# Kernel optimization log

Hardware: AMD Instinct MI355X
Metric: run time of the kernel (lower is better)

Reference implementation:

```python
import jax, jax.numpy as jnp
import numpy as np

NEG = -jnp.inf


def _pipeline(logits, presence_penalties, frequency_penalties, repetition_penalties,
              temperatures, top_p, min_p, top_a, tfs, typical_p,
              epsilon_cutoff, eta_cutoff, smoothing_factor, smoothing_curve,
              prompt_tokens, output_tokens, top_k):
    N, V = logits.shape
    rows = jnp.arange(N)[:, None]
    cols = jnp.arange(V)[None, :]

    # ---- presence / frequency / repetition penalties (bincount via scatter-add) ----
    pbin = jnp.zeros((N, V + 1), jnp.int32).at[rows, prompt_tokens].add(1)[:, :V]
    obin = jnp.zeros((N, V + 1), jnp.int32).at[rows, output_tokens].add(1)[:, :V]
    seen = (pbin > 0) | (obin > 0)
    rp = jnp.where(seen, repetition_penalties[:, None], 1.0)
    logits = jnp.where(logits > 0, logits / rp, logits * rp)
    logits = logits - frequency_penalties[:, None] * obin.astype(logits.dtype)
    logits = logits - presence_penalties[:, None] * (obin > 0).astype(logits.dtype)

    # ---- temperature ----
    logits = logits / temperatures[:, None]

    # ---- top-k + top-p (sort ascending, mask, unsort) ----
    order = jnp.argsort(logits, axis=-1)               # ascending
    ls = jnp.take_along_axis(logits, order, axis=-1)
    kth_pos = (V - jnp.clip(top_k.astype(jnp.int32), 1, V))[:, None]
    kth_val = jnp.take_along_axis(ls, kth_pos, axis=1)
    ls = jnp.where(ls < kth_val, NEG, ls)
    cs = jnp.cumsum(jax.nn.softmax(ls, axis=-1), axis=-1)
    pmask = (cs <= (1.0 - top_p)[:, None]).at[:, -1].set(False)
    ls = jnp.where(pmask, NEG, ls)
    logits = jnp.take_along_axis(ls, jnp.argsort(order, axis=-1), axis=-1)

    # ---- tail-free sampling (sort descending, 2nd-derivative CDF cutoff) ----
    order_d = jnp.argsort(-logits, axis=-1)            # descending order of logits
    ls = jnp.take_along_axis(logits, order_d, axis=-1)
    probs = jax.nn.softmax(ls, axis=-1)
    d2 = jnp.abs(jnp.diff(jnp.diff(probs, axis=-1), axis=-1))   # (N, V-2)
    cdf = jnp.cumsum(d2 / jnp.sum(d2, axis=-1, keepdims=True), axis=-1)
    m = cdf > tfs[:, None]
    m = jnp.concatenate([jnp.zeros((N, 1), bool), m, jnp.ones((N, 1), bool)], axis=-1)
    ls = jnp.where(m, NEG, ls)
    logits = jnp.take_along_axis(ls, jnp.argsort(order_d, axis=-1), axis=-1)

    # ---- eta cutoff (entropy-adaptive threshold, always keep argmax) ----
    sl = jax.nn.log_softmax(logits, axis=-1)
    probs = jnp.exp(sl)
    sl_safe = jnp.where(probs > 0, sl, 0.0)            # nansum equivalent
    neg_ent = jnp.sum(probs * sl_safe, axis=-1)
    eps = jnp.minimum(eta_cutoff, jnp.sqrt(eta_cutoff) * jnp.exp(neg_ent))[:, None]
    top_idx = jnp.argmax(probs, axis=-1)[:, None]
    logits = jnp.where((probs < eps) & (cols != top_idx), NEG, logits)

    # ---- epsilon cutoff (absolute prob threshold, always keep argmax) ----
    probs = jax.nn.softmax(logits, axis=-1)
    top_idx = jnp.argmax(probs, axis=-1)[:, None]
    logits = jnp.where((probs < epsilon_cutoff[:, None]) & (cols != top_idx), NEG, logits)

    # ---- locally typical sampling ----
    sl = jax.nn.log_softmax(logits, axis=-1)
    probs = jnp.exp(sl)
    sl_safe = jnp.where(probs > 0, sl, 0.0)
    neg_ent = jnp.sum(probs * sl_safe, axis=-1, keepdims=True)
    dev = jnp.abs(neg_ent - sl)                        # surprisal deviation
    order_t = jnp.argsort(dev, axis=-1)
    rp2 = jnp.take_along_axis(probs, order_t, axis=-1)
    msort = (jnp.cumsum(rp2, axis=-1) >= typical_p[:, None]).at[:, 0].set(False)
    mask = jnp.zeros((N, V), bool).at[rows, order_t].set(msort)
    logits = jnp.where(mask, NEG, logits)

    # ---- quadratic (smoothing) sampling ----
    mx = jnp.max(logits, axis=-1, keepdims=True)
    finite = logits != NEG
    diff = jnp.where(finite, logits, mx) - mx          # finite everywhere
    kq = (3.0 - smoothing_curve[:, None]) / 2.0
    sq = (smoothing_curve[:, None] - 1.0) / 2.0
    sfc = smoothing_factor[:, None]
    trans = -(kq * sfc * diff ** 2) + sq * sfc * diff ** 3 + mx
    trans = jnp.where(finite, trans, logits)
    logits = jnp.where(sfc > 0, trans, logits)

    # ---- min-p ----
    probs = jax.nn.softmax(logits, axis=-1)
    top_prob = jnp.max(probs, axis=-1, keepdims=True)
    logits = jnp.where(probs < min_p[:, None] * top_prob, NEG, logits)

    # ---- top-a ----
    probs = jax.nn.softmax(logits, axis=-1)
    top_prob = jnp.max(probs, axis=-1, keepdims=True)
    logits = jnp.where(probs < top_a[:, None] * top_prob ** 2, NEG, logits)

    return logits


def setup_inputs() -> dict:
    N, V, PL, OL = 256, 50257, 512, 128
    ks = jax.random.split(jax.random.key(0), 17)
    u = lambda k, lo, hi: lo + (hi - lo) * jax.random.uniform(k, (N,), jnp.float32)
    return {
        "logits": 3.0 * jax.random.normal(ks[0], (N, V), jnp.float32),
        "prompt_tokens": jax.random.randint(ks[1], (N, PL), 0, V),
        "output_tokens": jax.random.randint(ks[2], (N, OL), 0, V),
        "presence_penalties": u(ks[3], 0.0, 0.5),
        "frequency_penalties": u(ks[4], 0.0, 0.5),
        "repetition_penalties": u(ks[5], 1.0, 1.3),
        "temperatures": u(ks[6], 0.5, 1.5),
        "top_p": u(ks[7], 0.85, 0.99),
        "top_k": jax.random.randint(ks[8], (N,), 1, 2048, dtype=jnp.int32),
        "min_p": u(ks[9], 0.0, 0.05),
        "top_a": u(ks[10], 0.0, 0.1),
        "tfs": u(ks[11], 0.95, 0.999),
        "typical_p": u(ks[12], 0.9, 0.999),
        "epsilon_cutoff": u(ks[13], 1e-5, 1e-4),
        "eta_cutoff": u(ks[14], 1e-5, 1e-4),
        "smoothing_factor": u(ks[15], 0.05, 0.25),
        "smoothing_curve": u(ks[16], 1.0, 2.0),
    }


def reference(logits, prompt_tokens, output_tokens, presence_penalties,
              frequency_penalties, repetition_penalties, temperatures, top_p,
              top_k, min_p, top_a, tfs, typical_p, epsilon_cutoff, eta_cutoff,
              smoothing_factor, smoothing_curve):
    return _pipeline(logits, presence_penalties, frequency_penalties,
                     repetition_penalties, temperatures, top_p, min_p, top_a,
                     tfs, typical_p, epsilon_cutoff, eta_cutoff,
                     smoothing_factor, smoothing_curve,
                     prompt_tokens, output_tokens, top_k)
```

## Files before the change

### kernel.cpp

```cpp
#include <hip/hip_runtime.h>
#include <stdint.h>

#define TPB 1024
#define NWAVE 16
#define MAXK 2304
#define NV4 13
#define BIG_NEG (-1.0e30f)

__device__ __forceinline__ uint32_t fkey(float x) {
  uint32_t s = __float_as_uint(x);
  return (s & 0x80000000u) ? ~s : (s | 0x80000000u);
}
__device__ __forceinline__ float fkey_inv(uint32_t u) {
  uint32_t s = (u & 0x80000000u) ? (u & 0x7fffffffu) : ~u;
  return __uint_as_float(s);
}
__device__ __forceinline__ unsigned long long shfl_xor_u64(unsigned long long v, int m) {
  uint32_t lo = (uint32_t)v, hi = (uint32_t)(v >> 32);
  lo = (uint32_t)__shfl_xor((int)lo, m, 64);
  hi = (uint32_t)__shfl_xor((int)hi, m, 64);
  return (((unsigned long long)hi) << 32) | lo;
}

struct TokMem { uint32_t obin[12568]; uint32_t seen[1600]; };
struct SortMem { unsigned long long kp[4096]; };
union __align__(16) U1 { TokMem tok; SortMem srt; };

__device__ __forceinline__ float block_sum1(float v, float* buf) {
  int lane = threadIdx.x & 63, wd = threadIdx.x >> 6;
#pragma unroll
  for (int off = 32; off > 0; off >>= 1) v += __shfl_down(v, off, 64);
  if (lane == 0) buf[wd] = v;
  __syncthreads();
  const float4* b4 = (const float4*)buf;
  float4 A = b4[0], B = b4[1], C = b4[2], D = b4[3];
  float r = A.x; r += A.y; r += A.z; r += A.w;
  r += B.x; r += B.y; r += B.z; r += B.w;
  r += C.x; r += C.y; r += C.z; r += C.w;
  r += D.x; r += D.y; r += D.z; r += D.w;
  return r;
}
__device__ __forceinline__ int block_count(int c, float* buf) {
  return (int)block_sum1((float)c, buf);
}

__device__ __forceinline__ float wbuf_prefix(const float* wbuf, int wd) {
  const float4* w4 = (const float4*)wbuf;
  float4 a = w4[0], b = w4[1], c = w4[2], d = w4[3];
  float t[16] = {a.x, a.y, a.z, a.w, b.x, b.y, b.z, b.w,
                 c.x, c.y, c.z, c.w, d.x, d.y, d.z, d.w};
  float base = 0.f;
#pragma unroll
  for (int i = 0; i < 16; ++i) base += (i < wd) ? t[i] : 0.f;
  return base;
}

__device__ void block_scan3(float* arr, int m, float* wbuf) {
  int tid = (int)threadIdx.x, lane = tid & 63, wd = tid >> 6;
  int b = tid * 3;
  __syncthreads();
  float a0 = (b < m) ? arr[b] : 0.f;
  float a1 = (b + 1 < m) ? arr[b + 1] : 0.f;
  float a2 = (b + 2 < m) ? arr[b + 2] : 0.f;
  float c1 = a0 + a1, c2 = c1 + a2;
  float t = c2, w = c2;
#pragma unroll
  for (int off = 1; off < 64; off <<= 1) {
    float x = __shfl_up(w, off, 64);
    if (lane >= off) w += x;
  }
  if (lane == 63) wbuf[wd] = w;
  __syncthreads();
  float base = wbuf_prefix(wbuf, wd);
  float excl = base + (w - t);
  if (b < m) arr[b] = a0 + excl;
  if (b + 1 < m) arr[b + 1] = c1 + excl;
  if (b + 2 < m) arr[b + 2] = c2 + excl;
  __syncthreads();
}

__device__ void block_scan3x2(float* A, float* B, int m, float* wbufA, float* wbufB) {
  int tid = (int)threadIdx.x, lane = tid & 63, wd = tid >> 6;
  int b = tid * 3;
  __syncthreads();
  float a0 = (b < m) ? A[b] : 0.f;
  float a1 = (b + 1 < m) ? A[b + 1] : 0.f;
  float a2 = (b + 2 < m) ? A[b + 2] : 0.f;
  float x0 = (b < m) ? B[b] : 0.f;
  float x1 = (b + 1 < m) ? B[b + 1] : 0.f;
  float x2 = (b + 2 < m) ? B[b + 2] : 0.f;
  float ca1 = a0 + a1, ca2 = ca1 + a2;
  float cx1 = x0 + x1, cx2 = cx1 + x2;
  float ta = ca2, wa = ca2, tx = cx2, wx = cx2;
#pragma unroll
  for (int off = 1; off < 64; off <<= 1) {
    float sa = __shfl_up(wa, off, 64);
    float sx = __shfl_up(wx, off, 64);
    if (lane >= off) { wa += sa; wx += sx; }
  }
  if (lane == 63) { wbufA[wd] = wa; wbufB[wd] = wx; }
  __syncthreads();
  float baseA = wbuf_prefix(wbufA, wd);
  float baseB = wbuf_prefix(wbufB, wd);
  float exA = baseA + (wa - ta), exB = baseB + (wx - tx);
  if (b < m) { A[b] = a0 + exA; B[b] = x0 + exB; }
  if (b + 1 < m) { A[b + 1] = ca1 + exA; B[b + 1] = cx1 + exB; }
  if (b + 2 < m) { A[b + 2] = ca2 + exA; B[b + 2] = cx2 + exB; }
  __syncthreads();
}

__device__ uint32_t wave_select_digit2k(const uint32_t* __restrict__ h, uint32_t* w_io) {
  int lane = threadIdx.x & 63;
  uint32_t w = *w_io;
  const int base = lane << 5;
  uint32_t lsum = 0;
#pragma unroll
  for (int t = 0; t < 8; ++t) {
    const int tt = (t + lane) & 7;
    const uint4 v = *(const uint4*)(h + base + tt * 4);
    lsum += v.x + v.y + v.z + v.w;
  }
  uint32_t W = lsum;
#pragma unroll
  for (int off = 1; off < 64; off <<= 1) {
    uint32_t x = (uint32_t)__shfl_down((int)W, off, 64);
    if (lane + off < 64) W += x;
  }
  uint32_t Wn = (uint32_t)__shfl_down((int)W, 1, 64);
  if (lane == 63) Wn = 0;
  const bool isb = (W >= w) && (Wn < w);
  int dloc = -1; uint32_t wloc = 0;
  if (isb) {
    uint32_t sfx = Wn;
#pragma unroll
    for (int t = 31; t >= 0; --t) {
      uint32_t c = h[base + t];
      uint32_t si = sfx + c;
      if (si >= w && sfx < w) { dloc = base + t; wloc = w - sfx; }
      sfx = si;
    }
  }
  unsigned long long bm = __ballot(dloc >= 0);
  int src = (int)__popcll(bm - 1ull);
  uint32_t d = (uint32_t)__shfl(dloc, src, 64);
  *w_io = (uint32_t)__shfl((int)wloc, src, 64);
  return d;
}

__device__ uint32_t wave_select_digit256(const uint32_t* __restrict__ h, uint32_t* w_io) {
  int lane = threadIdx.x & 63;
  uint32_t w = *w_io;
  const uint4 v = ((const uint4*)h)[lane];
  uint32_t c0 = v.x, c1 = v.y, c2 = v.z, c3 = v.w;
  uint32_t t0 = c0 + c1 + c2 + c3;
  uint32_t W = t0;
#pragma unroll
  for (int off = 1; off < 64; off <<= 1) {
    uint32_t x = (uint32_t)__shfl_down((int)W, off, 64);
    if (lane + off < 64) W += x;
  }
  uint32_t Wn = (uint32_t)__shfl_down((int)W, 1, 64);
  if (lane == 63) Wn = 0;
  uint32_t S0 = W, S1 = W - c0, S2 = S1 - c1, S3 = S2 - c2, S4 = Wn;
  int dloc = -1; uint32_t wloc = 0;
  if (S0 >= w && S1 < w) { dloc = 4 * lane + 0; wloc = w - S1; }
  if (S1 >= w && S2 < w) { dloc = 4 * lane + 1; wloc = w - S2; }
  if (S2 >= w && S3 < w) { dloc = 4 * lane + 2; wloc = w - S3; }
  if (S3 >= w && S4 < w) { dloc = 4 * lane + 3; wloc = w - S4; }
  unsigned long long bm = __ballot(dloc >= 0);
  int src = (int)__popcll(bm - 1ull);
  uint32_t d = (uint32_t)__shfl(dloc, src, 64);
  *w_io = (uint32_t)__shfl((int)wloc, src, 64);
  return d;
}

template <int NE, bool PING>
__device__ void hybrid_sort(unsigned long long* kp, unsigned long long* kb1, int n) {
  const int tid = (int)threadIdx.x;
  unsigned long long k[NE];
#pragma unroll
  for (int e = 0; e < NE; ++e) {
    int i = e * TPB + tid;
    k[e] = (i < n) ? kp[i] : ~0ull;
  }
  int pb = 0;
  for (int kk = 2; kk <= n; kk <<= 1) {
    for (int j = kk >> 1; j > 0; j >>= 1) {
      if (j >= TPB) {
        const int em = j / TPB;
#pragma unroll
        for (int e = 0; e < NE; ++e) {
          if ((e & em) == 0 && (e + em) < NE) {
            int e2 = e + em;
            int i = e * TPB + tid;
            bool up = ((i & kk) == 0);
            if ((k[e] > k[e2]) == up) {
              unsigned long long tk = k[e]; k[e] = k[e2]; k[e2] = tk;
            }
          }
        }
      } else if (j >= 64) {
        unsigned long long* kb = (PING && pb) ? kb1 : kp;
#pragma unroll
        for (int e = 0; e < NE; ++e) {
          int i = e * TPB + tid;
          if (i < n) kb[i] = k[e];
        }
        __syncthreads();
#pragma unroll
        for (int e = 0; e < NE; ++e) {
          int i = e * TPB + tid;
          if (i < n) {
            unsigned long long o = kb[i ^ j];
            bool up = ((i & kk) == 0);
            bool lower = ((i & j) == 0);
            bool takeMin = (lower == up);
            bool takeOther = takeMin ? (o < k[e]) : (o > k[e]);
            if (takeOther) k[e] = o;
          }
        }
        if (PING) pb ^= 1;
        else __syncthreads();
      } else {
#pragma unroll
        for (int e = 0; e < NE; ++e) {
          int i = e * TPB + tid;
          unsigned long long o = shfl_xor_u64(k[e], j);
          bool up = ((i & kk) == 0);
          bool lower = ((i & j) == 0);
          bool takeMin = (lower == up);
          bool takeOther = takeMin ? (o < k[e]) : (o > k[e]);
          if (takeOther) k[e] = o;
        }
      }
    }
  }
  __syncthreads();
#pragma unroll
  for (int e = 0; e < NE; ++e) {
    int i = e * TPB + tid;
    if (i < n) kp[i] = k[e];
  }
  __syncthreads();
}

__device__ __forceinline__ uint32_t penal_val(float l, int j, bool sn,
    const uint32_t* __restrict__ obin,
    float f_rep, float inv_rep, float f_freq, float f_pres, float inv_temp) {
  int ob = 0;
  if (sn) ob = (int)((obin[j >> 2] >> (8 * (j & 3))) & 255u);
  l = (l > 0.0f) ? (l * (sn ? inv_rep : 1.0f)) : (l * (sn ? f_rep : 1.0f));
  l = l - f_freq * (float)ob;
  l = l - ((ob > 0) ? f_pres : 0.0f);
  l = l * inv_temp;
  return fkey(l);
}
__device__ __forceinline__ uint32_t penal_key(float l, int j,
    const uint32_t* __restrict__ seen, const uint32_t* __restrict__ obin,
    float f_rep, float inv_rep, float f_freq, float f_pres, float inv_temp) {
  bool sn = (seen[j >> 5] >> (j & 31)) & 1u;
  return penal_val(l, j, sn, obin, f_rep, inv_rep, f_freq, f_pres, inv_temp);
}

#define FOR_ELEMS(...) do {                                                   \
    if (tid < head) { int j = tid; uint32_t u = uh; (void)j; (void)u; __VA_ARGS__; } \
    _Pragma("unroll")                                                         \
    for (int s4_ = 0; s4_ < NV4; ++s4_) {                                     \
      int iv_ = s4_ * TPB + tid;                                              \
      if (iv_ < nvec) {                                                       \
        int jb_ = head + 4 * iv_;                                             \
        { int j = jb_ + 0; uint32_t u = uk[s4_ * 4 + 0]; (void)j; (void)u; __VA_ARGS__; } \
        { int j = jb_ + 1; uint32_t u = uk[s4_ * 4 + 1]; (void)j; (void)u; __VA_ARGS__; } \
        { int j = jb_ + 2; uint32_t u = uk[s4_ * 4 + 2]; (void)j; (void)u; __VA_ARGS__; } \
        { int j = jb_ + 3; uint32_t u = uk[s4_ * 4 + 3]; (void)j; (void)u; __VA_ARGS__; } \
      }                                                                       \
    }                                                                         \
    if (tid < ntail) { int j = head + 4 * nvec + tid; uint32_t u = ut; (void)j; (void)u; __VA_ARGS__; } \
  } while (0)

#define COLLECT_ELEM do {                                                     \
    bool pk_ = (u >= kth_u);                                                  \
    unsigned long long bm_ = __ballot(pk_);                                   \
    if (bm_) {                                                                \
      uint32_t base_ = 0;                                                     \
      if (lane == 0) base_ = atomicAdd(&s_cnt, (uint32_t)__popcll(bm_));      \
      base_ = (uint32_t)__shfl((int)base_, 0, 64);                            \
      if (pk_) {                                                              \
        uint32_t pos_ = base_ + (uint32_t)__popcll(bm_ & ((1ull << (unsigned)lane) - 1ull)); \
        if (pos_ < MAXK)                                                      \
          kp[pos_] = (((unsigned long long)(~u)) << 16) | (unsigned long long)(uint32_t)j; \
      }                                                                       \
    }                                                                         \
  } while (0)

__global__ __launch_bounds__(TPB, 4)
void sampler_kernel(const float* __restrict__ logits,
                    const int* __restrict__ ptoks, const int* __restrict__ otoks,
                    const float* __restrict__ pres, const float* __restrict__ freq,
                    const float* __restrict__ rep, const float* __restrict__ temp,
                    const float* __restrict__ topp, const int* __restrict__ topk,
                    const float* __restrict__ minp, const float* __restrict__ topa,
                    const float* __restrict__ tfsv, const float* __restrict__ typp,
                    const float* __restrict__ epsc, const float* __restrict__ etac,
                    const float* __restrict__ smf, const float* __restrict__ smc,
                    float* __restrict__ out, int N, int V, int PL, int OL) {
  __shared__ U1 u1;
  __shared__ __align__(16) uint32_t s_hist2k[2048];
  __shared__ __align__(16) uint32_t s_h256[256];
  __shared__ float s_e[MAXK];
  __shared__ float s_p[MAXK];
  __shared__ float s_q[MAXK];
  __shared__ float s_r[MAXK];
  __shared__ unsigned long long kb1[2048];
  __shared__ __align__(16) float s_site[12][NWAVE];
  __shared__ uint32_t s_cnt;
  __shared__ int s_ilo, s_ihi;

  const int tid = (int)threadIdx.x;
  const int r = (int)blockIdx.x;
  const int wd = tid >> 6;
  const int lane = tid & 63;

  const float* lrow = logits + (size_t)r * V;
  float* orow = out + (size_t)r * V;

  {
    const uint4 z4 = make_uint4(0u, 0u, 0u, 0u);
    uint4* ob4 = (uint4*)u1.tok.obin;
    for (int i = tid; i < 3142; i += TPB) ob4[i] = z4;
    uint4* se4 = (uint4*)u1.tok.seen;
    for (int i = tid; i < 400; i += TPB) se4[i] = z4;
    uint4* h4 = (uint4*)s_hist2k;
    for (int i = tid; i < 512; i += TPB) h4[i] = z4;
    if (tid < 64) ((uint4*)s_h256)[tid] = z4;
  }
  if (tid == 0) s_cnt = 0;
  __syncthreads();
  for (int i = tid; i < PL; i += TPB) {
    int t = ptoks[(size_t)r * PL + i];
    if ((unsigned)t < (unsigned)V) atomicOr(&u1.tok.seen[t >> 5], 1u << (t & 31));
  }
  for (int i = tid; i < OL; i += TPB) {
    int t = otoks[(size_t)r * OL + i];
    if ((unsigned)t < (unsigned)V) {
      atomicOr(&u1.tok.seen[t >> 5], 1u << (t & 31));
      atomicAdd(&u1.tok.obin[t >> 2], 1u << (8 * (t & 3)));
    }
  }
  __syncthreads();

  const float f_pres = pres[r], f_freq = freq[r], f_rep = rep[r], f_temp = temp[r];
  const float f_topp = topp[r], f_minp = minp[r], f_topa = topa[r], f_tfs = tfsv[r];
  const float f_typp = typp[r], f_epsc = epsc[r], f_etac = etac[r];
  const float f_smf = smf[r], f_smc = smc[r];
  const float inv_rep = 1.0f / f_rep, inv_temp = 1.0f / f_temp;
  int k_topk = topk[r];
  if (k_topk < 1) k_topk = 1;
  if (k_topk > V) k_topk = V;

  const uint32_t* seenp = u1.tok.seen;
  const uint32_t* obinp = u1.tok.obin;

  uintptr_t ra = (uintptr_t)lrow;
  int head = (int)(((16u - (uint32_t)(ra & 15u)) & 15u) >> 2);
  if (head > V) head = V;
  const int nvec = (V - head) >> 2;
  const int ntail = V - head - (nvec << 2);

  uint32_t uk[NV4 * 4];
  uint32_t uh = 0, ut = 0;
#pragma unroll
  for (int s4 = 0; s4 < NV4; ++s4) {
    int iv = s4 * TPB + tid;
    uint32_t u0 = 0, u1k = 0, u2k = 0, u3 = 0;
    if (iv < nvec) {
      const float4 lv = *(const float4*)(lrow + head + 4 * iv);
      int jb = head + 4 * iv;
      uint32_t w0 = seenp[jb >> 5];
      uint32_t w1 = seenp[(jb >> 5) + 1];
      uint32_t sb = (uint32_t)(((((uint64_t)w1) << 32) | (uint64_t)w0) >> (jb & 31));
      u0 = penal_val(lv.x, jb + 0, (sb >> 0) & 1u, obinp, f_rep, inv_rep, f_freq, f_pres, inv_temp);
      u1k = penal_val(lv.y, jb + 1, (sb >> 1) & 1u, obinp, f_rep, inv_rep, f_freq, f_pres, inv_temp);
      u2k = penal_val(lv.z, jb + 2, (sb >> 2) & 1u, obinp, f_rep, inv_rep, f_freq, f_pres, inv_temp);
      u3 = penal_val(lv.w, jb + 3, (sb >> 3) & 1u, obinp, f_rep, inv_rep, f_freq, f_pres, inv_temp);
      atomicAdd(&s_hist2k[u0 >> 21], 1u);
      atomicAdd(&s_hist2k[u1k >> 21], 1u);
      atomicAdd(&s_hist2k[u2k >> 21], 1u);
      atomicAdd(&s_hist2k[u3 >> 21], 1u);
    }
    uk[s4 * 4 + 0] = u0; uk[s4 * 4 + 1] = u1k; uk[s4 * 4 + 2] = u2k; uk[s4 * 4 + 3] = u3;
  }
  if (tid < head) {
    uh = penal_key(lrow[tid], tid, seenp, obinp, f_rep, inv_rep, f_freq, f_pres, inv_temp);
    atomicAdd(&s_hist2k[uh >> 21], 1u);
  }
  if (tid < ntail) {
    int j = head + 4 * nvec + tid;
    ut = penal_key(lrow[j], j, seenp, obinp, f_rep, inv_rep, f_freq, f_pres, inv_temp);
    atomicAdd(&s_hist2k[ut >> 21], 1u);
  }

  {
    uintptr_t oa = (uintptr_t)orow;
    int ohead = (int)(((16u - (uint32_t)(oa & 15u)) & 15u) >> 2);
    if (ohead > V) ohead = V;
    int onvec = (V - ohead) >> 2;
    for (int j = tid; j < ohead; j += TPB) orow[j] = BIG_NEG;
    float4* o4 = (float4*)(orow + ohead);
    const float4 f4 = make_float4(BIG_NEG, BIG_NEG, BIG_NEG, BIG_NEG);
    for (int i = tid; i < onvec; i += TPB) o4[i] = f4;
    for (int j = ohead + (onvec << 2) + tid; j < V; j += TPB) orow[j] = BIG_NEG;
  }
  __syncthreads();

  uint32_t w = (uint32_t)k_topk;
  uint32_t d11 = wave_select_digit2k(s_hist2k, &w);
  FOR_ELEMS(if ((u >> 21) == d11) atomicAdd(&s_h256[(u >> 13) & 255u], 1u));
  __syncthreads();
  uint32_t d8 = wave_select_digit256(s_h256, &w);
  const uint32_t kth_u = (d11 << 21) | (d8 << 13);

  unsigned long long* kp = u1.srt.kp;
  FOR_ELEMS(COLLECT_ELEM);
  __syncthreads();
  int K = (int)s_cnt;
  if (K > MAXK) K = MAXK;

  {
    int n1 = 64; while (n1 < K) n1 <<= 1;
    for (int i = K + tid; i < n1; i += TPB) kp[i] = ~0ull;
    __syncthreads();
    if (n1 <= 1024) hybrid_sort<1, true>(kp, kb1, n1);
    else if (n1 == 2048) hybrid_sort<2, true>(kp, kb1, n1);
    else hybrid_sort<4, false>(kp, nullptr, n1);
  }

  {
    const uint32_t kth_inv = (uint32_t)(kp[k_topk - 1] >> 16);
    int c = 0;
    for (int i = tid; i < K; i += TPB)
      if ((uint32_t)(kp[i] >> 16) <= kth_inv) c++;
    K = block_count(c, s_site[10]);
  }

  const float m0 = fkey_inv(~(uint32_t)(kp[0] >> 16));

  for (int i = tid; i < K; i += TPB) {
    float v = fkey_inv(~(uint32_t)(kp[i] >> 16));
    float e = __expf(v - m0);
    s_e[i] = e; s_p[i] = e; s_q[i] = e * (v - m0);
  }
  block_scan3x2(s_p, s_q, K, s_site[8], s_site[9]);
  const float S = s_p[K - 1];

  {
    const float thS = (1.0f - f_topp) * S;
    int c = 0;
    for (int i = tid; i < K; i += TPB) {
      float ss = S - s_p[i] + s_e[i];
      if (i == 0 || ss > thS) c++;
    }
    K = block_count(c, s_site[0]);
  }

  {
    for (int i = tid; i < K; i += TPB) {
      float e0 = s_e[i];
      float e1 = (i + 1 < K) ? s_e[i + 1] : 0.f;
      float e2 = (i + 2 < K) ? s_e[i + 2] : 0.f;
      s_r[i] = fabsf((e2 - e1) - (e1 - e0));
    }
    block_scan3(s_r, K, s_site[7]);
    const float thT = f_tfs * s_r[K - 1];
    int c = 0;
    for (int i = tid; i < K; i += TPB)
      if (i == 0 || s_r[i - 1] <= thT) c++;
    K = block_count(c, s_site[1]);
  }

  {
    const float SD = s_p[K - 1];
    const float ne = s_q[K - 1] / SD - __logf(SD);
    const float eps = fminf(f_etac, sqrtf(f_etac) * __expf(ne));
    const float thD = eps * SD;
    int c = 0;
    for (int i = tid; i < K; i += TPB)
      if (i == 0 || s_e[i] >= thD) c++;
    K = block_count(c, s_site[2]);
  }

  {
    const float thE = f_epsc * s_p[K - 1];
    int c = 0;
    for (int i = tid; i < K; i += TPB)
      if (i == 0 || s_e[i] >= thE) c++;
    K = block_count(c, s_site[3]);
  }

  int i_lo = 0, i_hi = K - 1;
  {
    const float SF = s_p[K - 1];
    const float lseF = __logf(SF);
    const float ne = s_q[K - 1] / SF - lseF;
    const float vth = ne + lseF + m0;
    const float typSF = f_typp * SF;
    int cc = 0;
    for (int i = tid; i < K; i += TPB)
      if (fkey_inv(~(uint32_t)(kp[i] >> 16)) >= vth) cc++;
    const int c = block_count(cc, s_site[4]);
    const int nB = K - c;

    if (wd == 0) {
      auto keyAt = [&](int i) -> unsigned long long {
        unsigned long long kk = kp[i];
        float v = fkey_inv(~(uint32_t)(kk >> 16));
        return (((unsigned long long)fkey(fabsf(v - vth))) << 16) | (kk & 0xffffull);
      };
      auto splitFor = [&](int p) -> int {
        int alo = p - nB; if (alo < 0) alo = 0;
        int ahi = (p < c) ? p : c;
        while (alo < ahi) {
          int am = (alo + ahi + 1) >> 1;
          int tb = p - am;
          bool take = true;
          if (tb < nB) take = (keyAt(c - am) <= keyAt(c + tb));
          if (take) alo = am; else ahi = am - 1;
        }
        return alo;
      };
      auto massLess = [&](int p) -> bool {
        int a = splitFor(p);
        int b = p - a;
        float sum = s_p[c + b - 1] - ((c - a > 0) ? s_p[c - a - 1] : 0.f);
        return sum < typSF;
      };
      int plo = 0, phi = K;
      while (phi > plo) {
        int range = phi - plo;
        int stride = (range + 63) >> 6;
        int p = plo + stride * (lane + 1);
        bool q = false;
        if (p <= phi) q = massLess(p);
        unsigned long long bm = __ballot(q);
        int h = bm ? (63 - (int)__clzll(bm)) : -1;
        int nlo = (h >= 0) ? (plo + stride * (h + 1)) : plo;
        long long nf = (long long)plo + (long long)stride * (long long)(h + 2);
        int nhi = (nf <= (long long)phi) ? (int)nf - 1 : phi;
        plo = nlo; phi = nhi;
      }
      int L = plo;
      if (L < 1) L = 1;
      if (L > K) L = K;
      int a = splitFor(L);
      if (lane == 0) { s_ilo = c - a; s_ihi = c + (L - a) - 1; }
    }
    __syncthreads();
    i_lo = s_ilo; i_hi = s_ihi;
  }

  float S2;
  const float mx = fkey_inv(~(uint32_t)(kp[i_lo] >> 16));
  {
    const float kq = (3.0f - f_smc) * 0.5f;
    const float sq = (f_smc - 1.0f) * 0.5f;
    float pS = 0.f;
    for (int i = i_lo + tid; i <= i_hi; i += TPB) {
      float v = fkey_inv(~(uint32_t)(kp[i] >> 16));
      float d = v - mx;
      float tr = mx - (kq * f_smf) * (d * d) + (sq * f_smf) * ((d * d) * d);
      float v2 = (f_smf > 0.0f) ? tr : v;
      float e = __expf(v2 - mx);
      s_q[i] = e;
      s_r[i] = v2;
      if (e >= f_minp) pS += e;
    }
    S2 = block_sum1(pS, s_site[6]);
  }

  {
    const float thA = f_topa / S2;
    for (int i = i_lo + tid; i <= i_hi; i += TPB) {
      float e = s_q[i];
      if (e >= f_minp && e >= thA) {
        int idx = (int)(kp[i] & 0xffffull);
        orow[idx] = s_r[i];
      }
    }
  }
}

extern "C" void kernel_launch(void* const* d_in, const int* in_sizes, int n_in,
                              void* d_out, int out_size, void* d_ws, size_t ws_size,
                              hipStream_t stream) {
  const float* logits = (const float*)d_in[0];
  const int* ptoks = (const int*)d_in[1];
  const int* otoks = (const int*)d_in[2];
  const float* pres = (const float*)d_in[3];
  const float* freq = (const float*)d_in[4];
  const float* rep  = (const float*)d_in[5];
  const float* temp = (const float*)d_in[6];
  const float* topp = (const float*)d_in[7];
  const int*   topk = (const int*)d_in[8];
  const float* minp = (const float*)d_in[9];
  const float* topa = (const float*)d_in[10];
  const float* tfsv = (const float*)d_in[11];
  const float* typp = (const float*)d_in[12];
  const float* epsc = (const float*)d_in[13];
  const float* etac = (const float*)d_in[14];
  const float* smf  = (const float*)d_in[15];
  const float* smc  = (const float*)d_in[16];

  int N = in_sizes[3];
  int V = in_sizes[0] / N;
  int PL = in_sizes[1] / N;
  int OL = in_sizes[2] / N;

  sampler_kernel<<<N, TPB, 0, stream>>>(logits, ptoks, otoks, pres, freq, rep, temp,
                                        topp, topk, minp, topa, tfsv, typp, epsc, etac,
                                        smf, smc, (float*)d_out, N, V, PL, OL);
}
```

Measured before the change: 70.51 us.

## Replace block-wide count reductions with single-wave parallel searches over sorted prefix sums

The cutoff stages (top-k tie count, top-p, tail-free, eta, epsilon, typical split point) were each block-wide count-and-reduce passes with barriers. They now run in one wave as 64-way parallel searches over the sorted prefix-sum arrays, relying on each cutoff predicate being monotone. The three prefix scans (exp, entropy term, TFS second difference) are fused into one scan. A third radix-select digit pass is added to narrow the top-k candidate set before sorting. This removes many __syncthreads and reductions, but puts serial work on a single wave, and the TFS cutoff now assumes its cumsum on the full-length array matches the one on the truncated array.

```diff
diff --git a/kernel.cpp b/kernel.cpp
--- a/kernel.cpp
+++ b/kernel.cpp
@@ -40,9 +40,6 @@
   r += D.x; r += D.y; r += D.z; r += D.w;
   return r;
 }
-__device__ __forceinline__ int block_count(int c, float* buf) {
-  return (int)block_sum1((float)c, buf);
-}
 
 __device__ __forceinline__ float wbuf_prefix(const float* wbuf, int wd) {
   const float4* w4 = (const float4*)wbuf;
@@ -55,57 +52,66 @@
   return base;
 }
 
-__device__ void block_scan3(float* arr, int m, float* wbuf) {
+__device__ __forceinline__ int wave_reduce_int(int v) {
+#pragma unroll
+  for (int off = 32; off > 0; off >>= 1) v += __shfl_down(v, off, 64);
+  return __shfl(v, 0, 64);
+}
+
+template <class Pred>
+__device__ __forceinline__ int wave_psearch(int lo, int hi, Pred pred) {
+  const int lane = (int)threadIdx.x & 63;
+  while (lo <= hi) {
+    int range = hi - lo + 1;
+    int stride = (range + 63) >> 6;
+    long long p = (long long)lo + (long long)stride * lane;
+    bool q = (p <= hi) ? pred((int)p) : false;
+    unsigned long long bm = __ballot(q);
+    int h = bm ? (63 - (int)__clzll(bm)) : -1;
+    int nlo = (h >= 0) ? (int)((long long)lo + (long long)stride * h + 1) : lo;
+    long long pf = (long long)lo + (long long)stride * (h + 1);
+    int nhi = (pf <= (long long)hi) ? (int)pf - 1 : hi;
+    if (nlo > nhi) return nlo;
+    lo = nlo; hi = nhi;
+  }
+  return lo;
+}
+
+__device__ void block_scan3x3(const float* __restrict__ se, float* __restrict__ sp,
+                              float* __restrict__ sq, float* __restrict__ sr, int m,
+                              float* wA, float* wB, float* wC) {
   int tid = (int)threadIdx.x, lane = tid & 63, wd = tid >> 6;
   int b = tid * 3;
   __syncthreads();
-  float a0 = (b < m) ? arr[b] : 0.f;
-  float a1 = (b + 1 < m) ? arr[b + 1] : 0.f;
-  float a2 = (b + 2 < m) ? arr[b + 2] : 0.f;
-  float c1 = a0 + a1, c2 = c1 + a2;
-  float t = c2, w = c2;
+  float e0 = (b     < m) ? se[b]     : 0.f;
+  float e1 = (b + 1 < m) ? se[b + 1] : 0.f;
+  float e2 = (b + 2 < m) ? se[b + 2] : 0.f;
+  float e3 = (b + 3 < m) ? se[b + 3] : 0.f;
+  float e4 = (b + 4 < m) ? se[b + 4] : 0.f;
+  float q0 = (b     < m) ? sq[b]     : 0.f;
+  float q1 = (b + 1 < m) ? sq[b + 1] : 0.f;
+  float q2 = (b + 2 < m) ? sq[b + 2] : 0.f;
+  float z0 = fabsf((e2 - e1) - (e1 - e0));
+  float z1 = fabsf((e3 - e2) - (e2 - e1));
+  float z2 = fabsf((e4 - e3) - (e3 - e2));
+  float ae1 = e0 + e1, ae2 = ae1 + e2;
+  float aq1 = q0 + q1, aq2 = aq1 + q2;
+  float az1 = z0 + z1, az2 = az1 + z2;
+  float tE = ae2, wE = ae2, tQ = aq2, wQ = aq2, tZ = az2, wZ = az2;
 #pragma unroll
   for (int off = 1; off < 64; off <<= 1) {
-    float x = __shfl_up(w, off, 64);
-    if (lane >= off) w += x;
-  }
-  if (lane == 63) wbuf[wd] = w;
-  __syncthreads();
-  float base = wbuf_prefix(wbuf, wd);
-  float excl = base + (w - t);
-  if (b < m) arr[b] = a0 + excl;
-  if (b + 1 < m) arr[b + 1] = c1 + excl;
-  if (b + 2 < m) arr[b + 2] = c2 + excl;
-  __syncthreads();
-}
-
-__device__ void block_scan3x2(float* A, float* B, int m, float* wbufA, float* wbufB) {
-  int tid = (int)threadIdx.x, lane = tid & 63, wd = tid >> 6;
-  int b = tid * 3;
-  __syncthreads();
-  float a0 = (b < m) ? A[b] : 0.f;
-  float a1 = (b + 1 < m) ? A[b + 1] : 0.f;
-  float a2 = (b + 2 < m) ? A[b + 2] : 0.f;
-  float x0 = (b < m) ? B[b] : 0.f;
-  float x1 = (b + 1 < m) ? B[b + 1] : 0.f;
-  float x2 = (b + 2 < m) ? B[b + 2] : 0.f;
-  float ca1 = a0 + a1, ca2 = ca1 + a2;
-  float cx1 = x0 + x1, cx2 = cx1 + x2;
-  float ta = ca2, wa = ca2, tx = cx2, wx = cx2;
-#pragma unroll
-  for (int off = 1; off < 64; off <<= 1) {
-    float sa = __shfl_up(wa, off, 64);
-    float sx = __shfl_up(wx, off, 64);
-    if (lane >= off) { wa += sa; wx += sx; }
-  }
-  if (lane == 63) { wbufA[wd] = wa; wbufB[wd] = wx; }
-  __syncthreads();
-  float baseA = wbuf_prefix(wbufA, wd);
-  float baseB = wbuf_prefix(wbufB, wd);
-  float exA = baseA + (wa - ta), exB = baseB + (wx - tx);
-  if (b < m) { A[b] = a0 + exA; B[b] = x0 + exB; }
-  if (b + 1 < m) { A[b + 1] = ca1 + exA; B[b + 1] = cx1 + exB; }
-  if (b + 2 < m) { A[b + 2] = ca2 + exA; B[b + 2] = cx2 + exB; }
+    float sE = __shfl_up(wE, off, 64);
+    float sQ = __shfl_up(wQ, off, 64);
+    float sZ = __shfl_up(wZ, off, 64);
+    if (lane >= off) { wE += sE; wQ += sQ; wZ += sZ; }
+  }
+  if (lane == 63) { wA[wd] = wE; wB[wd] = wQ; wC[wd] = wZ; }
+  __syncthreads();
+  float bE = wbuf_prefix(wA, wd), bQ = wbuf_prefix(wB, wd), bZ = wbuf_prefix(wC, wd);
+  float xE = bE + (wE - tE), xQ = bQ + (wQ - tQ), xZ = bZ + (wZ - tZ);
+  if (b < m)     { sp[b]     = e0 + xE;  sq[b]     = q0 + xQ;  sr[b]     = z0 + xZ; }
+  if (b + 1 < m) { sp[b + 1] = ae1 + xE; sq[b + 1] = aq1 + xQ; sr[b + 1] = az1 + xZ; }
+  if (b + 2 < m) { sp[b + 2] = ae2 + xE; sq[b + 2] = aq2 + xQ; sr[b + 2] = az2 + xZ; }
   __syncthreads();
 }
 
@@ -307,6 +313,7 @@
   __shared__ U1 u1;
   __shared__ __align__(16) uint32_t s_hist2k[2048];
   __shared__ __align__(16) uint32_t s_h256[256];
+  __shared__ __align__(16) uint32_t s_h256b[256];
   __shared__ float s_e[MAXK];
   __shared__ float s_p[MAXK];
   __shared__ float s_q[MAXK];
@@ -314,7 +321,7 @@
   __shared__ unsigned long long kb1[2048];
   __shared__ __align__(16) float s_site[12][NWAVE];
   __shared__ uint32_t s_cnt;
-  __shared__ int s_ilo, s_ihi;
+  __shared__ int s_K, s_ilo, s_ihi;
 
   const int tid = (int)threadIdx.x;
   const int r = (int)blockIdx.x;
@@ -333,6 +340,7 @@
     uint4* h4 = (uint4*)s_hist2k;
     for (int i = tid; i < 512; i += TPB) h4[i] = z4;
     if (tid < 64) ((uint4*)s_h256)[tid] = z4;
+    else if (tid >= 64 && tid < 128) ((uint4*)s_h256b)[tid - 64] = z4;
   }
   if (tid == 0) s_cnt = 0;
   __syncthreads();
@@ -418,7 +426,11 @@
   FOR_ELEMS(if ((u >> 21) == d11) atomicAdd(&s_h256[(u >> 13) & 255u], 1u));
   __syncthreads();
   uint32_t d8 = wave_select_digit256(s_h256, &w);
-  const uint32_t kth_u = (d11 << 21) | (d8 << 13);
+  const uint32_t pref19 = (d11 << 8) | d8;
+  FOR_ELEMS(if ((u >> 13) == pref19) atomicAdd(&s_h256b[(u >> 5) & 255u], 1u));
+  __syncthreads();
+  uint32_t d8c = wave_select_digit256(s_h256b, &w);
+  const uint32_t kth_u = (d11 << 21) | (d8 << 13) | (d8c << 5);
 
   unsigned long long* kp = u1.srt.kp;
   FOR_ELEMS(COLLECT_ELEM);
@@ -435,128 +447,120 @@
     else hybrid_sort<4, false>(kp, nullptr, n1);
   }
 
-  {
+  if (wd == 0) {
     const uint32_t kth_inv = (uint32_t)(kp[k_topk - 1] >> 16);
-    int c = 0;
-    for (int i = tid; i < K; i += TPB)
-      if ((uint32_t)(kp[i] >> 16) <= kth_inv) c++;
-    K = block_count(c, s_site[10]);
-  }
+    int KT = wave_psearch(0, K - 1, [&](int i) {
+      return (uint32_t)(kp[i] >> 16) <= kth_inv;
+    });
+    if (lane == 0) s_K = KT;
+  }
+  __syncthreads();
+  K = s_K;
 
   const float m0 = fkey_inv(~(uint32_t)(kp[0] >> 16));
 
   for (int i = tid; i < K; i += TPB) {
     float v = fkey_inv(~(uint32_t)(kp[i] >> 16));
     float e = __expf(v - m0);
-    s_e[i] = e; s_p[i] = e; s_q[i] = e * (v - m0);
-  }
-  block_scan3x2(s_p, s_q, K, s_site[8], s_site[9]);
-  const float S = s_p[K - 1];
-
-  {
+    s_e[i] = e; s_q[i] = e * (v - m0);
+  }
+  block_scan3x3(s_e, s_p, s_q, s_r, K, s_site[7], s_site[8], s_site[9]);
+
+  int i_lo = 0, i_hi = K - 1;
+  if (wd == 0) {
+    const float S = s_p[K - 1];
+
     const float thS = (1.0f - f_topp) * S;
-    int c = 0;
-    for (int i = tid; i < K; i += TPB) {
+    int cnt = 0;
+    for (int i = lane; i < K; i += 64) {
       float ss = S - s_p[i] + s_e[i];
-      if (i == 0 || ss > thS) c++;
-    }
-    K = block_count(c, s_site[0]);
-  }
-
-  {
-    for (int i = tid; i < K; i += TPB) {
-      float e0 = s_e[i];
-      float e1 = (i + 1 < K) ? s_e[i + 1] : 0.f;
-      float e2 = (i + 2 < K) ? s_e[i + 2] : 0.f;
-      s_r[i] = fabsf((e2 - e1) - (e1 - e0));
-    }
-    block_scan3(s_r, K, s_site[7]);
-    const float thT = f_tfs * s_r[K - 1];
-    int c = 0;
-    for (int i = tid; i < K; i += TPB)
-      if (i == 0 || s_r[i - 1] <= thT) c++;
-    K = block_count(c, s_site[1]);
-  }
-
-  {
-    const float SD = s_p[K - 1];
-    const float ne = s_q[K - 1] / SD - __logf(SD);
-    const float eps = fminf(f_etac, sqrtf(f_etac) * __expf(ne));
+      if (i == 0 || ss > thS) cnt++;
+    }
+    int K1 = wave_reduce_int(cnt);
+
+    auto dzAt = [&](int i, int mm) -> float {
+      float x0 = s_e[i];
+      float x1 = (i + 1 < mm) ? s_e[i + 1] : 0.f;
+      float x2 = (i + 2 < mm) ? s_e[i + 2] : 0.f;
+      return fabsf((x2 - x1) - (x1 - x0));
+    };
+    int K2;
+    if (K1 >= 2) {
+      float base = (K1 >= 3) ? s_r[K1 - 3] : 0.f;
+      float rKm2 = base + dzAt(K1 - 2, K1);
+      float rKm1 = rKm2 + dzAt(K1 - 1, K1);
+      const float thT = f_tfs * rKm1;
+      const int Km3 = K1 - 3;
+      K2 = 1 + wave_psearch(0, K1 - 2, [&](int j) {
+        float rj = (j <= Km3) ? s_r[j] : rKm2;
+        return rj <= thT;
+      });
+    } else K2 = 1;
+
+    const float SD = s_p[K2 - 1];
+    const float neD = s_q[K2 - 1] / SD - __logf(SD);
+    const float eps = fminf(f_etac, sqrtf(f_etac) * __expf(neD));
     const float thD = eps * SD;
-    int c = 0;
-    for (int i = tid; i < K; i += TPB)
-      if (i == 0 || s_e[i] >= thD) c++;
-    K = block_count(c, s_site[2]);
-  }
-
-  {
-    const float thE = f_epsc * s_p[K - 1];
-    int c = 0;
-    for (int i = tid; i < K; i += TPB)
-      if (i == 0 || s_e[i] >= thE) c++;
-    K = block_count(c, s_site[3]);
-  }
-
-  int i_lo = 0, i_hi = K - 1;
-  {
-    const float SF = s_p[K - 1];
+    int K3 = wave_psearch(1, K2 - 1, [&](int i) { return s_e[i] >= thD; });
+
+    const float thE = f_epsc * s_p[K3 - 1];
+    int K4 = wave_psearch(1, K3 - 1, [&](int i) { return s_e[i] >= thE; });
+
+    const float SF = s_p[K4 - 1];
     const float lseF = __logf(SF);
-    const float ne = s_q[K - 1] / SF - lseF;
-    const float vth = ne + lseF + m0;
+    const float neF = s_q[K4 - 1] / SF - lseF;
+    const float vth = neF + lseF + m0;
     const float typSF = f_typp * SF;
-    int cc = 0;
-    for (int i = tid; i < K; i += TPB)
-      if (fkey_inv(~(uint32_t)(kp[i] >> 16)) >= vth) cc++;
-    const int c = block_count(cc, s_site[4]);
-    const int nB = K - c;
-
-    if (wd == 0) {
-      auto keyAt = [&](int i) -> unsigned long long {
-        unsigned long long kk = kp[i];
-        float v = fkey_inv(~(uint32_t)(kk >> 16));
-        return (((unsigned long long)fkey(fabsf(v - vth))) << 16) | (kk & 0xffffull);
-      };
-      auto splitFor = [&](int p) -> int {
-        int alo = p - nB; if (alo < 0) alo = 0;
-        int ahi = (p < c) ? p : c;
-        while (alo < ahi) {
-          int am = (alo + ahi + 1) >> 1;
-          int tb = p - am;
-          bool take = true;
-          if (tb < nB) take = (keyAt(c - am) <= keyAt(c + tb));
-          if (take) alo = am; else ahi = am - 1;
-        }
-        return alo;
-      };
-      auto massLess = [&](int p) -> bool {
-        int a = splitFor(p);
-        int b = p - a;
-        float sum = s_p[c + b - 1] - ((c - a > 0) ? s_p[c - a - 1] : 0.f);
-        return sum < typSF;
-      };
-      int plo = 0, phi = K;
-      while (phi > plo) {
-        int range = phi - plo;
-        int stride = (range + 63) >> 6;
-        int p = plo + stride * (lane + 1);
-        bool q = false;
-        if (p <= phi) q = massLess(p);
-        unsigned long long bm = __ballot(q);
-        int h = bm ? (63 - (int)__clzll(bm)) : -1;
-        int nlo = (h >= 0) ? (plo + stride * (h + 1)) : plo;
-        long long nf = (long long)plo + (long long)stride * (long long)(h + 2);
-        int nhi = (nf <= (long long)phi) ? (int)nf - 1 : phi;
-        plo = nlo; phi = nhi;
+    const int c = wave_psearch(0, K4 - 1, [&](int i) {
+      return fkey_inv(~(uint32_t)(kp[i] >> 16)) >= vth;
+    });
+    const int nB = K4 - c;
+
+    auto keyAt = [&](int i) -> unsigned long long {
+      unsigned long long kk = kp[i];
+      float v = fkey_inv(~(uint32_t)(kk >> 16));
+      return (((unsigned long long)fkey(fabsf(v - vth))) << 16) | (kk & 0xffffull);
+    };
+    auto splitFor = [&](int p) -> int {
+      int alo = p - nB; if (alo < 0) alo = 0;
+      int ahi = (p < c) ? p : c;
+      while (alo < ahi) {
+        int am = (alo + ahi + 1) >> 1;
+        int tb = p - am;
+        bool take = true;
+        if (tb < nB) take = (keyAt(c - am) <= keyAt(c + tb));
+        if (take) alo = am; else ahi = am - 1;
       }
-      int L = plo;
-      if (L < 1) L = 1;
-      if (L > K) L = K;
-      int a = splitFor(L);
-      if (lane == 0) { s_ilo = c - a; s_ihi = c + (L - a) - 1; }
-    }
-    __syncthreads();
-    i_lo = s_ilo; i_hi = s_ihi;
-  }
+      return alo;
+    };
+    auto massLess = [&](int p) -> bool {
+      int a = splitFor(p);
+      int b = p - a;
+      float sum = s_p[c + b - 1] - ((c - a > 0) ? s_p[c - a - 1] : 0.f);
+      return sum < typSF;
+    };
+    int plo = 0, phi = K4;
+    while (phi > plo) {
+      int range = phi - plo;
+      int stride = (range + 63) >> 6;
+      int p = plo + stride * (lane + 1);
+      bool q = false;
+      if (p <= phi) q = massLess(p);
+      unsigned long long bm = __ballot(q);
+      int h = bm ? (63 - (int)__clzll(bm)) : -1;
+      int nlo = (h >= 0) ? (plo + stride * (h + 1)) : plo;
+      long long nf = (long long)plo + (long long)stride * (long long)(h + 2);
+      int nhi = (nf <= (long long)phi) ? (int)nf - 1 : phi;
+      plo = nlo; phi = nhi;
+    }
+    int L = plo;
+    if (L < 1) L = 1;
+    if (L > K4) L = K4;
+    int a = splitFor(L);
+    if (lane == 0) { s_ilo = c - a; s_ihi = c + (L - a) - 1; }
+  }
+  __syncthreads();
+  i_lo = s_ilo; i_hi = s_ihi;
 
   float S2;
   const float mx = fkey_inv(~(uint32_t)(kp[i_lo] >> 16));
```

Result: slower. 72.67 us (+3.1%).
